# Kernel tuning notes

Measured on AMD Instinct MI355X. Metric: run time of the kernel, lower is better.

Reference implementation:

```python
import jax, jax.numpy as jnp
import numpy as np

T = 4      # num_step (also LSTM num_layers)
R = 64     # num_relation (= LSTM hidden size)
E = 1024   # num_entity
B = 128    # batch
IN = R + 2 * E  # LSTM input size


def _lstm_layer(x_seq, Wih, Whh, bih, bhh):
    # x_seq: [T, B, In]; torch gate order i, f, g, o
    Bsz = x_seq.shape[1]
    H = Whh.shape[1]
    pre = jnp.einsum('tbi,gi->tbg', x_seq, Wih) + bih + bhh  # [T,B,4H]

    def step(carry, z):
        h, c = carry
        z = z + h @ Whh.T
        i, f, g, o = jnp.split(z, 4, axis=-1)
        i, f, o = jax.nn.sigmoid(i), jax.nn.sigmoid(f), jax.nn.sigmoid(o)
        c = f * c + i * jnp.tanh(g)
        h = o * jnp.tanh(c)
        return (h, c), h

    init = (jnp.zeros((Bsz, H), x_seq.dtype), jnp.zeros((Bsz, H), x_seq.dtype))
    _, hs = jax.lax.scan(step, init, pre)
    return hs  # [T, B, H]


def setup_inputs() -> dict:
    key = jax.random.key(0)
    ks = jax.random.split(key, 12)
    s = 0.05
    inp = {
        'x': jax.random.uniform(ks[0], (B, IN), dtype=jnp.float32),
        'kb': jax.random.uniform(ks[1], (R, E, E), dtype=jnp.float32) * 0.01,
        # LSTM layer 0 (input dim IN)
        'Wih0': jax.random.normal(ks[2], (4 * R, IN), dtype=jnp.float32) * s,
        'Whh0': jax.random.normal(ks[3], (4 * R, R), dtype=jnp.float32) * s,
        'bih0': jnp.zeros((4 * R,), jnp.float32),
        'bhh0': jnp.zeros((4 * R,), jnp.float32),
        # LSTM layers 1..T-1 (input dim R)
        'Wih': jax.random.normal(ks[4], (T - 1, 4 * R, R), dtype=jnp.float32) * s,
        'Whh': jax.random.normal(ks[5], (T - 1, 4 * R, R), dtype=jnp.float32) * s,
        'bih': jnp.zeros((T - 1, 4 * R), jnp.float32),
        'bhh': jnp.zeros((T - 1, 4 * R), jnp.float32),
    }
    return inp


def reference(x, kb, Wih0, Whh0, bih0, bhh0, Wih, Whh, bih, bhh):
    # input to LSTM: x repeated T times -> [T, B, IN]
    seq = jnp.broadcast_to(x[None], (T,) + x.shape)
    hs = _lstm_layer(seq, Wih0, Whh0, bih0, bhh0)
    for l in range(T - 1):  # small fixed layer count
        hs = _lstm_layer(hs, Wih[l], Whh[l], bih[l], bhh[l])
    h = jax.nn.softmax(hs, axis=-1)  # [T, B, R] (first softmax)

    mem = [x[:, R:R + E]]  # memory[0] = head entity vector, [B, E]
    for i in range(T):
        h2 = jax.nn.softmax(h[i], axis=-1)  # double softmax, faithful to source
        # causal memory attention over steps k <= i
        att = jax.nn.softmax(jnp.einsum('kbr,br->bk', h[:i + 1], h[i]), axis=-1)  # [B, i+1]
        prev = jnp.einsum('bk,kbe->be', att, jnp.stack(mem))  # [B, E]
        # per-relation operator application: sum_r h2[b,r] * KB[r] @ prev[b]
        tmp = jnp.einsum('ref,bf->bre', kb, prev)  # [B, R, E]
        mem.append(jnp.einsum('br,bre->be', h2, tmp))

    tail = x[:, R + E:R + 2 * E]  # [B, E]
    score = jax.nn.sigmoid(-jnp.einsum('be,be->b', mem[-1], tail))[:, None]  # [B, 1]
    return score
```

## Files before the change

kernel.cpp:

```cpp
#include <hip/hip_runtime.h>
#include <cstdint>
#include <cstddef>

#define B_ 128
#define E_ 1024
#define R_ 64
#define T_ 4
#define IN_ 2112
#define G_ 256

typedef __attribute__((ext_vector_type(4))) float f32x4;
typedef __attribute__((ext_vector_type(8))) __bf16 bf16x8;

__device__ __forceinline__ unsigned short f2bf(float f) {
  unsigned int u = __float_as_uint(f);
  u += 0x7fffu + ((u >> 16) & 1u);
  return (unsigned short)(u >> 16);
}
__device__ __forceinline__ unsigned int pack2(float lo, float hi) {
  return (unsigned int)f2bf(lo) | ((unsigned int)f2bf(hi) << 16);
}
__device__ __forceinline__ float wred_sum(float v) {
#pragma unroll
  for (int m = 32; m > 0; m >>= 1) v += __shfl_xor(v, m, 64);
  return v;
}
__device__ __forceinline__ float wred_max(float v) {
#pragma unroll
  for (int m = 32; m > 0; m >>= 1) v = fmaxf(v, __shfl_xor(v, m, 64));
  return v;
}
__device__ __forceinline__ float sigmoidf_(float x) { return 1.f / (1.f + expf(-x)); }
__device__ __forceinline__ float fast_sig(float x) {
  return __builtin_amdgcn_rcpf(1.f + __expf(-x));
}
__device__ __forceinline__ float fast_tanh(float x) {
  return 1.f - 2.f * __builtin_amdgcn_rcpf(1.f + __expf(2.f * x));
}

__device__ __forceinline__ void gload_lds16(const void* g, void* l) {
  __builtin_amdgcn_global_load_lds(
      (const __attribute__((address_space(1))) unsigned int*)g,
      (__attribute__((address_space(3))) unsigned int*)l, 16, 0, 0);
}

__global__ __launch_bounds__(256, 2) void head_kernel(
    const float* __restrict__ x, const float* __restrict__ kb,
    const float* __restrict__ Wih0, const float* __restrict__ Whh0,
    const float* __restrict__ bih0, const float* __restrict__ bhh0,
    const float* __restrict__ Wih, const float* __restrict__ Whh,
    const float* __restrict__ bih, const float* __restrict__ bhh,
    unsigned short* __restrict__ kb_bf,
    float* __restrict__ h2_out, float* __restrict__ att_out,
    unsigned short* __restrict__ prev_bf) {
  const int tid = threadIdx.x;

  if (blockIdx.x >= 128) {
    const size_t base = (size_t)(blockIdx.x - 128) * 8192;
#pragma unroll
    for (int c = 0; c < 4; c++) {
      size_t o = base + (size_t)c * 2048 + (size_t)tid * 8;
      float4 v0 = *(const float4*)(kb + o);
      float4 v1 = *(const float4*)(kb + o + 4);
      uint4 u;
      u.x = pack2(v0.x, v0.y); u.y = pack2(v0.z, v0.w);
      u.z = pack2(v1.x, v1.y); u.w = pack2(v1.z, v1.w);
      *(uint4*)(kb_bf + o) = u;
    }
    return;
  }

  __shared__ __align__(16) float xrow[IN_];
  __shared__ __align__(16) float pre_lds[G_];
  __shared__ __align__(16) float hbuf[R_];
  __shared__ __align__(16) float zbuf[2][G_];
  __shared__ __align__(16) float hs_out[T_][R_];
  __shared__ __align__(16) float hmat[T_][R_];

  const int b = blockIdx.x;
  const int lane = tid & 63, wv = tid >> 6;
  const int s = tid & 63;

  for (int l = tid; l < IN_; l += 256) xrow[l] = x[b * IN_ + l];
  __syncthreads();

  {
    const int gbase = wv * 64;
#pragma unroll 2
    for (int gg = 0; gg < 64; gg++) {
      const float* wr = Wih0 + (size_t)(gbase + gg) * IN_;
      float4 s4 = {0.f, 0.f, 0.f, 0.f};
#pragma unroll
      for (int k = 0; k < 8; k++) {
        float4 w = *(const float4*)(wr + (lane + 64 * k) * 4);
        float4 xv = *(const float4*)(&xrow[(lane + 64 * k) * 4]);
        s4.x += w.x * xv.x; s4.y += w.y * xv.y;
        s4.z += w.z * xv.z; s4.w += w.w * xv.w;
      }
      float part = (s4.x + s4.y) + (s4.z + s4.w);
      part += wr[2048 + lane] * xrow[2048 + lane];
      float tot = wred_sum(part);
      if (lane == 0) pre_lds[gbase + gg] = tot;
    }
  }
  float p0 = pre_lds[tid] + bih0[tid] + bhh0[tid];

  float4 w4[16];
  float pret[T_];

  auto scan = [&]() {
    __syncthreads();
    hbuf[s] = 0.f;
    float creg = 0.f;
#pragma unroll
    for (int t = 0; t < T_; t++) {
      float z0 = pret[t], z1 = 0.f, z2 = 0.f, z3 = 0.f;
#pragma unroll
      for (int q = 0; q < 16; q += 4) {
        float4 h0 = *(const float4*)(&hbuf[q * 4]);
        float4 h1 = *(const float4*)(&hbuf[q * 4 + 4]);
        float4 h2v = *(const float4*)(&hbuf[q * 4 + 8]);
        float4 h3 = *(const float4*)(&hbuf[q * 4 + 12]);
        z0 += h0.x * w4[q].x + h0.y * w4[q].y + h0.z * w4[q].z + h0.w * w4[q].w;
        z1 += h1.x * w4[q + 1].x + h1.y * w4[q + 1].y + h1.z * w4[q + 1].z + h1.w * w4[q + 1].w;
        z2 += h2v.x * w4[q + 2].x + h2v.y * w4[q + 2].y + h2v.z * w4[q + 2].z + h2v.w * w4[q + 2].w;
        z3 += h3.x * w4[q + 3].x + h3.y * w4[q + 3].y + h3.z * w4[q + 3].z + h3.w * w4[q + 3].w;
      }
      zbuf[t & 1][tid] = (z0 + z1) + (z2 + z3);
      __syncthreads();
      float iv = fast_sig(zbuf[t & 1][s]);
      float fv = fast_sig(zbuf[t & 1][R_ + s]);
      float gv = fast_tanh(zbuf[t & 1][2 * R_ + s]);
      float ov = fast_sig(zbuf[t & 1][3 * R_ + s]);
      creg = fv * creg + iv * gv;
      float h = ov * fast_tanh(creg);
      hbuf[s] = h;
      hs_out[t][s] = h;
    }
  };

#pragma unroll
  for (int t = 0; t < T_; t++) pret[t] = p0;
#pragma unroll
  for (int q = 0; q < 16; q++)
    w4[q] = *(const float4*)(Whh0 + (size_t)tid * R_ + q * 4);
  scan();

  for (int l = 0; l < T_ - 1; l++) {
#pragma unroll
    for (int q = 0; q < 16; q++)
      w4[q] = *(const float4*)(Wih + ((size_t)l * G_ + tid) * R_ + q * 4);
    const float bsum = bih[l * G_ + tid] + bhh[l * G_ + tid];
#pragma unroll
    for (int t = 0; t < T_; t++) {
      float p = bsum;
#pragma unroll
      for (int q = 0; q < 16; q++) {
        float4 hv = *(const float4*)(&hs_out[t][q * 4]);
        p += hv.x * w4[q].x + hv.y * w4[q].y + hv.z * w4[q].z + hv.w * w4[q].w;
      }
      pret[t] = p;
    }
#pragma unroll
    for (int q = 0; q < 16; q++)
      w4[q] = *(const float4*)(Whh + ((size_t)l * G_ + tid) * R_ + q * 4);
    scan();
  }

  {
    float v = hs_out[wv][lane];
    float mx = wred_max(v);
    float ev = expf(v - mx);
    float sm = wred_sum(ev);
    float hval = ev / sm;
    hmat[wv][lane] = hval;
    float mx2 = wred_max(hval);
    float e2 = expf(hval - mx2);
    float s2 = wred_sum(e2);
    h2_out[(wv * B_ + b) * R_ + lane] = e2 / s2;
    __syncthreads();
    float dots[T_];
    for (int k = 0; k <= wv; k++)
      dots[k] = wred_sum(hmat[k][lane] * hmat[wv][lane]);
    if (lane == 0) {
      float mx3 = dots[0];
      for (int k = 1; k <= wv; k++) mx3 = fmaxf(mx3, dots[k]);
      float ss = 0.f, es[T_];
      for (int k = 0; k <= wv; k++) { es[k] = expf(dots[k] - mx3); ss += es[k]; }
      for (int k = 0; k <= wv; k++) att_out[(wv * B_ + b) * 4 + k] = es[k] / ss;
    }
  }

  for (int l = tid; l < E_; l += 256)
    prev_bf[b * E_ + l] = f2bf(xrow[R_ + l]);
}

__global__ __launch_bounds__(256) void gemm_bf_kernel(
    const unsigned short* __restrict__ Abf,
    const unsigned short* __restrict__ Kbf,
    float* __restrict__ part) {
  __shared__ unsigned short As[2][128 * 32];
  __shared__ unsigned short Bs[2][128 * 32];
  const int tid = threadIdx.x, wv = tid >> 6, lane = tid & 63;
  const int et = blockIdx.x, r = blockIdx.y;
  const int wm = (wv & 1) * 64, wn = (wv >> 1) * 64;
  const int fr = lane & 15, koff = (lane >> 4) * 8;

  const int srow = wv * 32 + (lane >> 2);
  const int scol = (lane & 3) * 8;
  const unsigned short* agp = Abf + (size_t)srow * 1024 + scol;
  const unsigned short* bgp = Kbf + (size_t)r * 1048576 + (size_t)(et * 128 + srow) * 1024 + scol;

  f32x4 acc[4][4];
#pragma unroll
  for (int mt = 0; mt < 4; mt++)
#pragma unroll
    for (int nt = 0; nt < 4; nt++)
#pragma unroll
      for (int q = 0; q < 4; q++) acc[mt][nt][q] = 0.f;

  auto stage = [&](int buf, int kk) {
    gload_lds16(agp + kk * 32,             As[buf] + wv * 1024);
    gload_lds16(agp + kk * 32 + 16 * 1024, As[buf] + wv * 1024 + 512);
    gload_lds16(bgp + kk * 32,             Bs[buf] + wv * 1024);
    gload_lds16(bgp + kk * 32 + 16 * 1024, Bs[buf] + wv * 1024 + 512);
  };

  stage(0, 0);
  __syncthreads();
  int cur = 0;
  for (int kk = 0; kk < 32; kk++) {
    if (kk < 31) stage(cur ^ 1, kk + 1);
    bf16x8 af[4], bfr[4];
#pragma unroll
    for (int mt = 0; mt < 4; mt++)
      af[mt] = *(const bf16x8*)(As[cur] + (wm + mt * 16 + fr) * 32 + koff);
#pragma unroll
    for (int nt = 0; nt < 4; nt++)
      bfr[nt] = *(const bf16x8*)(Bs[cur] + (wn + nt * 16 + fr) * 32 + koff);
#pragma unroll
    for (int mt = 0; mt < 4; mt++)
#pragma unroll
      for (int nt = 0; nt < 4; nt++)
        acc[mt][nt] = __builtin_amdgcn_mfma_f32_16x16x32_bf16(af[mt], bfr[nt], acc[mt][nt], 0, 0, 0);
    __syncthreads();
    cur ^= 1;
  }
  const int crow = (lane >> 4) * 4;
  float* pout = part + (size_t)r * 131072;
#pragma unroll
  for (int mt = 0; mt < 4; mt++)
#pragma unroll
    for (int nt = 0; nt < 4; nt++)
#pragma unroll
      for (int q = 0; q < 4; q++)
        pout[(wm + mt * 16 + crow + q) * 1024 + et * 128 + wn + nt * 16 + fr] = acc[mt][nt][q];
}

__global__ __launch_bounds__(256) void mid_kernel(
    const float* __restrict__ part, const float* __restrict__ h2,
    const float* __restrict__ att, const float* __restrict__ x,
    float* __restrict__ mem, unsigned short* __restrict__ prev_bf, int it) {
  const int idx = blockIdx.x * 256 + threadIdx.x;
  const int b = idx >> 10, e = idx & 1023;
  const float* h2row = h2 + (it * B_ + b) * R_;
  const float* pp = part + idx;
  float s = 0.f;
#pragma unroll 8
  for (int rr = 0; rr < 64; rr++) s += h2row[rr] * pp[(size_t)rr * 131072];
  mem[it * 131072 + idx] = s;
  if (it < 3) {
    const float* arow = att + ((it + 1) * B_ + b) * 4;
    float acc = arow[0] * x[b * IN_ + R_ + e];
    for (int k = 1; k <= it; k++) acc += arow[k] * mem[(k - 1) * 131072 + idx];
    acc += arow[it + 1] * s;
    prev_bf[idx] = f2bf(acc);
  }
}

__global__ __launch_bounds__(256) void prep_fp32_kernel(
    const float* __restrict__ x, const float* __restrict__ att,
    const float* __restrict__ mem, float* __restrict__ prev,
    float* __restrict__ newmem, int it) {
  const int idx = blockIdx.x * 256 + threadIdx.x;
  const int b = idx >> 10, e = idx & 1023;
  const float* arow = att + (it * B_ + b) * 4;
  float acc = arow[0] * x[b * IN_ + R_ + e];
  for (int k = 1; k <= it; k++)
    acc += arow[k] * mem[(k - 1) * (B_ * E_) + b * E_ + e];
  prev[idx] = acc;
  newmem[idx] = 0.f;
}

__global__ __launch_bounds__(256) void gemm_fp32_kernel(
    const float* __restrict__ prev, const float* __restrict__ h2,
    const float* __restrict__ kb, float* __restrict__ out) {
  __shared__ unsigned short As[128 * 40];
  __shared__ unsigned short Bs[128 * 40];
  __shared__ float h2s[128];
  const int tid = threadIdx.x;
  const int et = blockIdx.x;
  const int r = blockIdx.y;
  if (tid < 128) h2s[tid] = h2[tid * 64 + r];
  __syncthreads();
  const int row = tid >> 1;
  const int c0 = (tid & 1) * 16;
  const float hsc = h2s[row];
  const float* aptr = prev + row * 1024 + c0;
  const float* bptr = kb + (size_t)r * (1024u * 1024u) + (size_t)(et * 128 + row) * 1024 + c0;
  unsigned short* adst = As + row * 40 + c0;
  unsigned short* bdst = Bs + row * 40 + c0;
  const int wv = tid >> 6, lane = tid & 63;
  const int wm = (wv & 1) * 64, wn = (wv >> 1) * 64;
  const int fr = lane & 15, koff = (lane >> 4) * 8;
  f32x4 acc[4][4];
#pragma unroll
  for (int mt = 0; mt < 4; mt++)
#pragma unroll
    for (int nt = 0; nt < 4; nt++)
#pragma unroll
      for (int q = 0; q < 4; q++) acc[mt][nt][q] = 0.f;
  for (int kk = 0; kk < 32; kk++) {
    const float4 a0 = *(const float4*)(aptr + kk * 32);
    const float4 a1 = *(const float4*)(aptr + kk * 32 + 4);
    const float4 a2 = *(const float4*)(aptr + kk * 32 + 8);
    const float4 a3 = *(const float4*)(aptr + kk * 32 + 12);
    const float4 b0 = *(const float4*)(bptr + kk * 32);
    const float4 b1 = *(const float4*)(bptr + kk * 32 + 4);
    const float4 b2 = *(const float4*)(bptr + kk * 32 + 8);
    const float4 b3 = *(const float4*)(bptr + kk * 32 + 12);
    __syncthreads();
    uint4 u;
    u.x = pack2(a0.x * hsc, a0.y * hsc); u.y = pack2(a0.z * hsc, a0.w * hsc);
    u.z = pack2(a1.x * hsc, a1.y * hsc); u.w = pack2(a1.z * hsc, a1.w * hsc);
    *(uint4*)adst = u;
    u.x = pack2(a2.x * hsc, a2.y * hsc); u.y = pack2(a2.z * hsc, a2.w * hsc);
    u.z = pack2(a3.x * hsc, a3.y * hsc); u.w = pack2(a3.z * hsc, a3.w * hsc);
    *(uint4*)(adst + 8) = u;
    u.x = pack2(b0.x, b0.y); u.y = pack2(b0.z, b0.w);
    u.z = pack2(b1.x, b1.y); u.w = pack2(b1.z, b1.w);
    *(uint4*)bdst = u;
    u.x = pack2(b2.x, b2.y); u.y = pack2(b2.z, b2.w);
    u.z = pack2(b3.x, b3.y); u.w = pack2(b3.z, b3.w);
    *(uint4*)(bdst + 8) = u;
    __syncthreads();
    bf16x8 af[4], bfr[4];
#pragma unroll
    for (int mt = 0; mt < 4; mt++)
      af[mt] = *(const bf16x8*)(As + (wm + mt * 16 + fr) * 40 + koff);
#pragma unroll
    for (int nt = 0; nt < 4; nt++)
      bfr[nt] = *(const bf16x8*)(Bs + (wn + nt * 16 + fr) * 40 + koff);
#pragma unroll
    for (int mt = 0; mt < 4; mt++)
#pragma unroll
      for (int nt = 0; nt < 4; nt++)
        acc[mt][nt] = __builtin_amdgcn_mfma_f32_16x16x32_bf16(af[mt], bfr[nt], acc[mt][nt], 0, 0, 0);
  }
  const int crow = (lane >> 4) * 4;
  const int ccol = et * 128 + fr;
#pragma unroll
  for (int mt = 0; mt < 4; mt++)
#pragma unroll
    for (int nt = 0; nt < 4; nt++)
#pragma unroll
      for (int q = 0; q < 4; q++)
        atomicAdd(&out[(wm + mt * 16 + crow + q) * 1024 + ccol + wn + nt * 16], acc[mt][nt][q]);
}

__global__ __launch_bounds__(256) void score_kernel(
    const float* __restrict__ x, const float* __restrict__ mem4,
    float* __restrict__ out) {
  __shared__ float red[4];
  const int b = blockIdx.x, tid = threadIdx.x;
  float s = 0.f;
  for (int e = tid; e < E_; e += 256)
    s += mem4[b * E_ + e] * x[b * IN_ + R_ + E_ + e];
  s = wred_sum(s);
  if ((tid & 63) == 0) red[tid >> 6] = s;
  __syncthreads();
  if (tid == 0) {
    float t = red[0] + red[1] + red[2] + red[3];
    out[b] = 1.f / (1.f + expf(t));
  }
}

extern "C" void kernel_launch(void* const* d_in, const int* in_sizes, int n_in,
                              void* d_out, int out_size, void* d_ws, size_t ws_size,
                              hipStream_t stream) {
  const float* x    = (const float*)d_in[0];
  const float* kb   = (const float*)d_in[1];
  const float* Wih0 = (const float*)d_in[2];
  const float* Whh0 = (const float*)d_in[3];
  const float* bih0 = (const float*)d_in[4];
  const float* bhh0 = (const float*)d_in[5];
  const float* Wih  = (const float*)d_in[6];
  const float* Whh  = (const float*)d_in[7];
  const float* bih  = (const float*)d_in[8];
  const float* bhh  = (const float*)d_in[9];

  float* ws    = (float*)d_ws;
  float* h2    = ws;
  float* att   = ws + 32768;
  float* mem   = ws + 34816;
  float* prevb = ws + 559104;
  float* part  = ws + 690176;
  float* kbbf  = ws + 9078784;
  const size_t need_big = (size_t)(9078784 + 33554432) * sizeof(float);
  const bool big = ws_size >= need_big;

  if (big) {
    head_kernel<<<8320, 256, 0, stream>>>(x, kb, Wih0, Whh0, bih0, bhh0,
                                          Wih, Whh, bih, bhh,
                                          (unsigned short*)kbbf, h2, att,
                                          (unsigned short*)prevb);
    for (int i = 0; i < 4; i++) {
      gemm_bf_kernel<<<dim3(8, 64), 256, 0, stream>>>(
          (const unsigned short*)prevb, (const unsigned short*)kbbf, part);
      mid_kernel<<<512, 256, 0, stream>>>(part, h2, att, x, mem,
                                          (unsigned short*)prevb, i);
    }
  } else {
    head_kernel<<<128, 256, 0, stream>>>(x, kb, Wih0, Whh0, bih0, bhh0,
                                         Wih, Whh, bih, bhh,
                                         (unsigned short*)prevb , h2, att,
                                         (unsigned short*)prevb);
    for (int i = 0; i < 4; i++) {
      float* newmem = mem + i * (B_ * E_);
      prep_fp32_kernel<<<512, 256, 0, stream>>>(x, att, mem, prevb, newmem, i);
      gemm_fp32_kernel<<<dim3(8, 64), 256, 0, stream>>>(prevb, h2 + i * (B_ * R_), kb, newmem);
    }
  }
  score_kernel<<<128, 256, 0, stream>>>(x, mem + 3 * (B_ * E_), (float*)d_out);
}
```

Measured before the change: 627.4 us.

## Fuse first-step bf16 GEMM with kb conversion into LSTM head kernel

The head kernel's conversion blocks now also run the step-0 GEMM: they load fp32 kb tiles and the head-entity slice of x, pack them to bf16 into LDS, write the bf16 kb copy out, and compute MFMA partials directly. This removes the separate step-0 gemm launch and the re-read of bf16 kb for that step, and runs the GEMM alongside the LSTM blocks. In exchange, the conversion blocks do unpipelined global loads with two barriers per k-step, and the shared LDS footprint changes occupancy for the LSTM blocks.

```diff
diff --git a/kernel.cpp b/kernel.cpp
--- a/kernel.cpp
+++ b/kernel.cpp
@@ -30,7 +30,6 @@
   for (int m = 32; m > 0; m >>= 1) v = fmaxf(v, __shfl_xor(v, m, 64));
   return v;
 }
-__device__ __forceinline__ float sigmoidf_(float x) { return 1.f / (1.f + expf(-x)); }
 __device__ __forceinline__ float fast_sig(float x) {
   return __builtin_amdgcn_rcpf(1.f + __expf(-x));
 }
@@ -44,40 +43,102 @@
       (__attribute__((address_space(3))) unsigned int*)l, 16, 0, 0);
 }
 
-__global__ __launch_bounds__(256, 2) void head_kernel(
+__global__ __launch_bounds__(256) void fused0_kernel(
     const float* __restrict__ x, const float* __restrict__ kb,
     const float* __restrict__ Wih0, const float* __restrict__ Whh0,
     const float* __restrict__ bih0, const float* __restrict__ bhh0,
     const float* __restrict__ Wih, const float* __restrict__ Whh,
     const float* __restrict__ bih, const float* __restrict__ bhh,
     unsigned short* __restrict__ kb_bf,
-    float* __restrict__ h2_out, float* __restrict__ att_out,
-    unsigned short* __restrict__ prev_bf) {
+    float* __restrict__ part,
+    float* __restrict__ h2_out, float* __restrict__ att_out) {
+  __shared__ __align__(16) unsigned char smem[20480];
   const int tid = threadIdx.x;
-
-  if (blockIdx.x >= 128) {
-    const size_t base = (size_t)(blockIdx.x - 128) * 8192;
-#pragma unroll
-    for (int c = 0; c < 4; c++) {
-      size_t o = base + (size_t)c * 2048 + (size_t)tid * 8;
-      float4 v0 = *(const float4*)(kb + o);
-      float4 v1 = *(const float4*)(kb + o + 4);
+  const int bid = blockIdx.x;
+
+  if (bid >= 128) {
+    unsigned short* As = (unsigned short*)smem;
+    unsigned short* Bs = As + 128 * 40;
+    const int g = bid - 128;
+    const int et = g & 7, r = g >> 3;
+    const int row = tid >> 1;
+    const int c0 = (tid & 1) * 16;
+    const float* aptr = x + (size_t)row * IN_ + R_ + c0;
+    const float* bptr = kb + (size_t)r * 1048576 + (size_t)(et * 128 + row) * 1024 + c0;
+    unsigned short* kdst = kb_bf + (size_t)r * 1048576 + (size_t)(et * 128 + row) * 1024 + c0;
+    unsigned short* adst = As + row * 40 + c0;
+    unsigned short* bdst = Bs + row * 40 + c0;
+    const int wv = tid >> 6, lane = tid & 63;
+    const int wm = (wv & 1) * 64, wn = (wv >> 1) * 64;
+    const int fr = lane & 15, koff = (lane >> 4) * 8;
+    f32x4 acc[4][4];
+#pragma unroll
+    for (int mt = 0; mt < 4; mt++)
+#pragma unroll
+      for (int nt = 0; nt < 4; nt++)
+#pragma unroll
+        for (int q = 0; q < 4; q++) acc[mt][nt][q] = 0.f;
+
+    for (int kk = 0; kk < 32; kk++) {
+      const float4 a0 = *(const float4*)(aptr + kk * 32);
+      const float4 a1 = *(const float4*)(aptr + kk * 32 + 4);
+      const float4 a2 = *(const float4*)(aptr + kk * 32 + 8);
+      const float4 a3 = *(const float4*)(aptr + kk * 32 + 12);
+      const float4 b0 = *(const float4*)(bptr + kk * 32);
+      const float4 b1 = *(const float4*)(bptr + kk * 32 + 4);
+      const float4 b2 = *(const float4*)(bptr + kk * 32 + 8);
+      const float4 b3 = *(const float4*)(bptr + kk * 32 + 12);
+      __syncthreads();
       uint4 u;
-      u.x = pack2(v0.x, v0.y); u.y = pack2(v0.z, v0.w);
-      u.z = pack2(v1.x, v1.y); u.w = pack2(v1.z, v1.w);
-      *(uint4*)(kb_bf + o) = u;
-    }
+      u.x = pack2(a0.x, a0.y); u.y = pack2(a0.z, a0.w);
+      u.z = pack2(a1.x, a1.y); u.w = pack2(a1.z, a1.w);
+      *(uint4*)adst = u;
+      u.x = pack2(a2.x, a2.y); u.y = pack2(a2.z, a2.w);
+      u.z = pack2(a3.x, a3.y); u.w = pack2(a3.z, a3.w);
+      *(uint4*)(adst + 8) = u;
+      uint4 ub;
+      ub.x = pack2(b0.x, b0.y); ub.y = pack2(b0.z, b0.w);
+      ub.z = pack2(b1.x, b1.y); ub.w = pack2(b1.z, b1.w);
+      *(uint4*)bdst = ub;
+      *(uint4*)(kdst + kk * 32) = ub;
+      ub.x = pack2(b2.x, b2.y); ub.y = pack2(b2.z, b2.w);
+      ub.z = pack2(b3.x, b3.y); ub.w = pack2(b3.z, b3.w);
+      *(uint4*)(bdst + 8) = ub;
+      *(uint4*)(kdst + kk * 32 + 8) = ub;
+      __syncthreads();
+      bf16x8 af[4], bfr[4];
+#pragma unroll
+      for (int mt = 0; mt < 4; mt++)
+        af[mt] = *(const bf16x8*)(As + (wm + mt * 16 + fr) * 40 + koff);
+#pragma unroll
+      for (int nt = 0; nt < 4; nt++)
+        bfr[nt] = *(const bf16x8*)(Bs + (wn + nt * 16 + fr) * 40 + koff);
+#pragma unroll
+      for (int mt = 0; mt < 4; mt++)
+#pragma unroll
+        for (int nt = 0; nt < 4; nt++)
+          acc[mt][nt] = __builtin_amdgcn_mfma_f32_16x16x32_bf16(af[mt], bfr[nt], acc[mt][nt], 0, 0, 0);
+    }
+    const int crow = (lane >> 4) * 4;
+    float* pout = part + (size_t)r * 131072;
+#pragma unroll
+    for (int mt = 0; mt < 4; mt++)
+#pragma unroll
+      for (int nt = 0; nt < 4; nt++)
+#pragma unroll
+        for (int q = 0; q < 4; q++)
+          pout[(wm + mt * 16 + crow + q) * 1024 + et * 128 + wn + nt * 16 + fr] = acc[mt][nt][q];
     return;
   }
 
-  __shared__ __align__(16) float xrow[IN_];
-  __shared__ __align__(16) float pre_lds[G_];
-  __shared__ __align__(16) float hbuf[R_];
-  __shared__ __align__(16) float zbuf[2][G_];
-  __shared__ __align__(16) float hs_out[T_][R_];
-  __shared__ __align__(16) float hmat[T_][R_];
-
-  const int b = blockIdx.x;
+  float* xrow    = (float*)smem;
+  float* pre_lds = xrow + IN_;
+  float* hbuf    = pre_lds + G_;
+  float* zbuf    = hbuf + R_;
+  float* hs_out  = zbuf + 2 * G_;
+  float* hmat    = hs_out + T_ * R_;
+
+  const int b = bid;
   const int lane = tid & 63, wv = tid >> 6;
   const int s = tid & 63;
 
@@ -97,9 +158,9 @@
         s4.x += w.x * xv.x; s4.y += w.y * xv.y;
         s4.z += w.z * xv.z; s4.w += w.w * xv.w;
       }
-      float part = (s4.x + s4.y) + (s4.z + s4.w);
-      part += wr[2048 + lane] * xrow[2048 + lane];
-      float tot = wred_sum(part);
+      float part_ = (s4.x + s4.y) + (s4.z + s4.w);
+      part_ += wr[2048 + lane] * xrow[2048 + lane];
+      float tot = wred_sum(part_);
       if (lane == 0) pre_lds[gbase + gg] = tot;
     }
   }
@@ -126,16 +187,16 @@
         z2 += h2v.x * w4[q + 2].x + h2v.y * w4[q + 2].y + h2v.z * w4[q + 2].z + h2v.w * w4[q + 2].w;
         z3 += h3.x * w4[q + 3].x + h3.y * w4[q + 3].y + h3.z * w4[q + 3].z + h3.w * w4[q + 3].w;
       }
-      zbuf[t & 1][tid] = (z0 + z1) + (z2 + z3);
+      zbuf[(t & 1) * G_ + tid] = (z0 + z1) + (z2 + z3);
       __syncthreads();
-      float iv = fast_sig(zbuf[t & 1][s]);
-      float fv = fast_sig(zbuf[t & 1][R_ + s]);
-      float gv = fast_tanh(zbuf[t & 1][2 * R_ + s]);
-      float ov = fast_sig(zbuf[t & 1][3 * R_ + s]);
+      float iv = fast_sig(zbuf[(t & 1) * G_ + s]);
+      float fv = fast_sig(zbuf[(t & 1) * G_ + R_ + s]);
+      float gv = fast_tanh(zbuf[(t & 1) * G_ + 2 * R_ + s]);
+      float ov = fast_sig(zbuf[(t & 1) * G_ + 3 * R_ + s]);
       creg = fv * creg + iv * gv;
       float h = ov * fast_tanh(creg);
       hbuf[s] = h;
-      hs_out[t][s] = h;
+      hs_out[t * R_ + s] = h;
     }
   };
 
@@ -156,7 +217,7 @@
       float p = bsum;
 #pragma unroll
       for (int q = 0; q < 16; q++) {
-        float4 hv = *(const float4*)(&hs_out[t][q * 4]);
+        float4 hv = *(const float4*)(&hs_out[t * R_ + q * 4]);
         p += hv.x * w4[q].x + hv.y * w4[q].y + hv.z * w4[q].z + hv.w * w4[q].w;
       }
       pret[t] = p;
@@ -168,12 +229,12 @@
   }
 
   {
-    float v = hs_out[wv][lane];
+    float v = hs_out[wv * R_ + lane];
     float mx = wred_max(v);
     float ev = expf(v - mx);
     float sm = wred_sum(ev);
     float hval = ev / sm;
-    hmat[wv][lane] = hval;
+    hmat[wv * R_ + lane] = hval;
     float mx2 = wred_max(hval);
     float e2 = expf(hval - mx2);
     float s2 = wred_sum(e2);
@@ -181,7 +242,7 @@
     __syncthreads();
     float dots[T_];
     for (int k = 0; k <= wv; k++)
-      dots[k] = wred_sum(hmat[k][lane] * hmat[wv][lane]);
+      dots[k] = wred_sum(hmat[k * R_ + lane] * hmat[wv * R_ + lane]);
     if (lane == 0) {
       float mx3 = dots[0];
       for (int k = 1; k <= wv; k++) mx3 = fmaxf(mx3, dots[k]);
@@ -190,9 +251,6 @@
       for (int k = 0; k <= wv; k++) att_out[(wv * B_ + b) * 4 + k] = es[k] / ss;
     }
   }
-
-  for (int l = tid; l < E_; l += 256)
-    prev_bf[b * E_ + l] = f2bf(xrow[R_ + l]);
 }
 
 __global__ __launch_bounds__(256) void gemm_bf_kernel(
@@ -410,21 +468,21 @@
   const bool big = ws_size >= need_big;
 
   if (big) {
-    head_kernel<<<8320, 256, 0, stream>>>(x, kb, Wih0, Whh0, bih0, bhh0,
-                                          Wih, Whh, bih, bhh,
-                                          (unsigned short*)kbbf, h2, att,
-                                          (unsigned short*)prevb);
-    for (int i = 0; i < 4; i++) {
+    fused0_kernel<<<640, 256, 0, stream>>>(x, kb, Wih0, Whh0, bih0, bhh0,
+                                           Wih, Whh, bih, bhh,
+                                           (unsigned short*)kbbf, part, h2, att);
+    mid_kernel<<<512, 256, 0, stream>>>(part, h2, att, x, mem,
+                                        (unsigned short*)prevb, 0);
+    for (int i = 1; i < 4; i++) {
       gemm_bf_kernel<<<dim3(8, 64), 256, 0, stream>>>(
           (const unsigned short*)prevb, (const unsigned short*)kbbf, part);
       mid_kernel<<<512, 256, 0, stream>>>(part, h2, att, x, mem,
                                           (unsigned short*)prevb, i);
     }
   } else {
-    head_kernel<<<128, 256, 0, stream>>>(x, kb, Wih0, Whh0, bih0, bhh0,
-                                         Wih, Whh, bih, bhh,
-                                         (unsigned short*)prevb , h2, att,
-                                         (unsigned short*)prevb);
+    fused0_kernel<<<128, 256, 0, stream>>>(x, kb, Wih0, Whh0, bih0, bhh0,
+                                           Wih, Whh, bih, bhh,
+                                           (unsigned short*)prevb, mem, h2, att);
     for (int i = 0; i < 4; i++) {
       float* newmem = mem + i * (B_ * E_);
       prep_fp32_kernel<<<512, 256, 0, stream>>>(x, att, mem, prevb, newmem, i);
```

Result: faster. 609.4 us (-2.9%).
